# Performance work log

Hardware: AMD Instinct MI355X
Metric: run time of the kernel (lower is better)

Reference implementation:

```python
import jax, jax.numpy as jnp
import numpy as np


def setup_inputs() -> dict:
    key = jax.random.key(0)
    ks = jax.random.split(key, 7)
    B, T, C, H = 4, 4096, 1024, 64
    x = jax.random.normal(ks[0], (B, T, C), dtype=jnp.float32)
    Wq = jax.random.normal(ks[1], (C, H), dtype=jnp.float32) * 0.02
    bq = jax.random.normal(ks[2], (H,), dtype=jnp.float32) * 0.02
    Wk = jax.random.normal(ks[3], (C, H), dtype=jnp.float32) * 0.02
    bk = jax.random.normal(ks[4], (H,), dtype=jnp.float32) * 0.02
    Wv = jax.random.normal(ks[5], (C, H), dtype=jnp.float32) * 0.02
    bv = jax.random.normal(ks[6], (H,), dtype=jnp.float32) * 0.02
    return {"x": x, "Wq": Wq, "bq": bq, "Wk": Wk, "bk": bk, "Wv": Wv, "bv": bv}


def reference(x, Wq, bq, Wk, bk, Wv, bv):
    B, T, C = x.shape
    q = x @ Wq + bq            # [B,T,H]
    k = x @ Wk + bk            # [B,T,H]
    v = x @ Wv + bv            # [B,T,H]
    # NOTE: original scales by C**-0.5 where C = n_embd (input dim), not head_size
    scale = jnp.asarray(C, x.dtype) ** -0.5
    wei = jnp.einsum('bth,bsh->bts', q, k) * scale   # [B,T,T]
    causal = jnp.tril(jnp.ones((T, T), dtype=bool))
    wei = jnp.where(causal, wei, -jnp.inf)
    wei = jax.nn.softmax(wei, axis=-1)
    out = jnp.einsum('bts,bsh->bth', wei, v)         # [B,T,H]
    return out
```

## Files before the change

### kernel.cpp

```cpp
#include <hip/hip_runtime.h>
#include <hip/hip_bf16.h>

#define T_DIM 4096
#define C_DIM 1024
#define H_DIM 64
#define B_DIM 4

typedef __attribute__((ext_vector_type(8))) short short8v;
typedef __attribute__((ext_vector_type(4))) short short4v;
typedef __attribute__((ext_vector_type(4))) float float4v;

__device__ __forceinline__ unsigned short f2bf(float f) {
    __hip_bfloat16 h = __float2bfloat16(f);
    return *reinterpret_cast<unsigned short*>(&h);
}
__device__ __forceinline__ float bf2f(unsigned short u) {
    __hip_bfloat16 h = *reinterpret_cast<__hip_bfloat16*>(&u);
    return __bfloat162float(h);
}

__device__ __forceinline__ int vperm(int t5) {
    return ((t5 & 12) << 1) | (t5 & 3) | ((t5 & 16) >> 2);
}

#define GLL16(gsrc, ldst)                                                         \
    __builtin_amdgcn_global_load_lds(                                             \
        (const __attribute__((address_space(1))) unsigned int*)(gsrc),            \
        (__attribute__((address_space(3))) unsigned int*)(ldst), 16, 0, 0)

__global__ __launch_bounds__(256) void wprep(
    const float* __restrict__ Wq, const float* __restrict__ Wk,
    const float* __restrict__ Wv, unsigned short* __restrict__ wt)
{
    const int tid = blockIdx.x * 256 + threadIdx.x;
    const int k   = tid & 1023;
    const int col = (tid >> 10) & 63;
    const int m   = tid >> 16;
    const float* __restrict__ W = (m == 0) ? Wq : (m == 1) ? Wk : Wv;
    wt[tid] = f2bf(W[k * 64 + col]);
}

__global__ __launch_bounds__(512, 2) void qkv_gemm(
    const float* __restrict__ x, const unsigned short* __restrict__ wt,
    const float* __restrict__ bq, const float* __restrict__ bk,
    const float* __restrict__ bv,
    unsigned short* __restrict__ qb, unsigned short* __restrict__ kmat,
    unsigned short* __restrict__ vP)
{
    __shared__ __align__(16) unsigned char lx[2][16384];
    __shared__ __align__(16) unsigned char lw[2][24576];

    const int t    = threadIdx.x;
    const int w    = t >> 6;
    const int lane = t & 63;
    const int l15  = lane & 15;
    const int g    = lane >> 4;
    const int r0   = blockIdx.x * 64;

    const int xgl = (t & 15) ^ ((t >> 4) & 15);
    const int wgl = (t & 7) ^ ((t >> 3) & 7);

    const unsigned char* __restrict__ xB = (const unsigned char*)x;
    const unsigned char* __restrict__ wB = (const unsigned char*)wt;

#define STAGE(p, kb)                                                              \
    {                                                                             \
        _Pragma("unroll")                                                         \
        for (int i = 0; i < 2; ++i) {                                             \
            const unsigned char* src =                                            \
                xB + (size_t)(r0 + i * 32 + (t >> 4)) * 4096 + (kb) * 256 + xgl * 16; \
            GLL16(src, &lx[p][(i * 512 + t) * 16]);                               \
        }                                                                         \
        _Pragma("unroll")                                                         \
        for (int j = 0; j < 3; ++j) {                                             \
            const unsigned char* src =                                            \
                wB + (size_t)(j * 64 + (t >> 3)) * 2048 + (kb) * 128 + wgl * 16;  \
            GLL16(src, &lw[p][(j * 512 + t) * 16]);                               \
        }                                                                         \
    }

    const int rbase = (w & 3) * 16;
    const int W0    = (w >> 2) * 96;

    float4v acc[6];
#pragma unroll
    for (int cg = 0; cg < 6; ++cg) acc[cg] = (float4v){0.f, 0.f, 0.f, 0.f};

    STAGE(0, 0);
    __syncthreads();

    for (int kb = 0; kb < 16; ++kb) {
        const int p = kb & 1;
        if (kb < 15) STAGE(p ^ 1, kb + 1);

        const int arow = rbase + l15;
        short8v af[2];
#pragma unroll
        for (int ks = 0; ks < 2; ++ks) {
            const int Lg0 = ks * 8 + 2 * g;
            const float4 a0 = *(const float4*)&lx[p][arow * 256 + ((Lg0)     ^ l15) * 16];
            const float4 a1 = *(const float4*)&lx[p][arow * 256 + ((Lg0 + 1) ^ l15) * 16];
            short8v a;
            a[0] = (short)f2bf(a0.x); a[1] = (short)f2bf(a0.y);
            a[2] = (short)f2bf(a0.z); a[3] = (short)f2bf(a0.w);
            a[4] = (short)f2bf(a1.x); a[5] = (short)f2bf(a1.y);
            a[6] = (short)f2bf(a1.z); a[7] = (short)f2bf(a1.w);
            af[ks] = a;
        }

#pragma unroll
        for (int cg = 0; cg < 6; ++cg) {
            const int wrow = W0 + cg * 16 + l15;
#pragma unroll
            for (int ks = 0; ks < 2; ++ks) {
                const int phys = (ks * 4 + g) ^ (l15 & 7);
                const short8v bf = *(const short8v*)&lw[p][wrow * 128 + phys * 16];
                acc[cg] = __builtin_amdgcn_mfma_f32_16x16x32_bf16(af[ks], bf, acc[cg], 0, 0, 0);
            }
        }
        __syncthreads();
    }

    const float qs = 0.03125f * 1.44269504088896f;
#pragma unroll
    for (int cg = 0; cg < 6; ++cg) {
        const int cabs = W0 + cg * 16 + l15;
        const int m    = cabs >> 6;
        const int h    = cabs & 63;
        const float bb = ((m == 0) ? bq : (m == 1) ? bk : bv)[h];
#pragma unroll
        for (int rr = 0; rr < 4; ++rr) {
            const int row = r0 + rbase + 4 * g + rr;
            const float vv = acc[cg][rr] + bb;
            if (m == 0) {
                qb[(size_t)row * 64 + h] = f2bf(vv * qs);
            } else if (m == 1) {
                kmat[(size_t)row * 64 + h] = f2bf(vv);
            } else {
                const int b_i = row >> 12;
                const int tt  = row & 4095;
                const int tp  = (tt & ~31) | vperm(tt & 31);
                vP[((size_t)b_i * 64 + h) * T_DIM + tp] = f2bf(vv);
            }
        }
    }
#undef STAGE
}

__global__ __launch_bounds__(512, 4) void attn_mfma(
    const unsigned short* __restrict__ qb, const unsigned short* __restrict__ kmat,
    const unsigned short* __restrict__ vP, float* __restrict__ out)
{
    __shared__ float partO[8][32][68];
    __shared__ float partl[8][32];

    const int w    = threadIdx.x >> 6;
    const int lane = threadIdx.x & 63;
    const int l15  = lane & 15;
    const int g    = lane >> 4;
    const int i    = blockIdx.x;
    const int p2   = (i & 255) >> 2;
    const int b    = i & 3;
    const int tt   = (i < 256) ? (127 - p2) : p2;
    const int q0   = tt * 32;
    const int n    = tt + 1;

    const unsigned short* __restrict__ qbase = qb + ((size_t)b * T_DIM + q0) * 64;
    short8v qf[2][2];
    qf[0][0] = *(const short8v*)(qbase + (size_t)l15 * 64 + 8 * g);
    qf[0][1] = *(const short8v*)(qbase + (size_t)l15 * 64 + 32 + 8 * g);
    qf[1][0] = *(const short8v*)(qbase + (size_t)(16 + l15) * 64 + 8 * g);
    qf[1][1] = *(const short8v*)(qbase + (size_t)(16 + l15) * 64 + 32 + 8 * g);

    const unsigned short* __restrict__ kbase = kmat + (size_t)b * T_DIM * 64;
    const unsigned short* __restrict__ vbase = vP + (size_t)b * 64 * T_DIM;

    float4v acc[2][4];
#pragma unroll
    for (int qt = 0; qt < 2; ++qt)
#pragma unroll
        for (int f = 0; f < 4; ++f) acc[qt][f] = (float4v){0.f, 0.f, 0.f, 0.f};
    float lsum[2] = {0.f, 0.f};

    const int rem = n & 7;
    const int cnt = (n >> 3) + (w < rem ? 1 : 0);
    const int st  = w * (n >> 3) + (w < rem ? w : rem);

    for (int s = 0; s < cnt; ++s) {
        const int kv0 = (st + s) * 32;

        const unsigned short* kr0 = kbase + (size_t)(kv0 + l15) * 64 + 8 * g;
        const unsigned short* kr1 = kr0 + 16 * 64;
        const short8v ka0 = *(const short8v*)kr0;
        const short8v ka1 = *(const short8v*)(kr0 + 32);
        const short8v ka2 = *(const short8v*)kr1;
        const short8v ka3 = *(const short8v*)(kr1 + 32);

        short8v vb4[4];
#pragma unroll
        for (int f = 0; f < 4; ++f)
            vb4[f] = *(const short8v*)(
                vbase + (size_t)(f * 16 + l15) * T_DIM + kv0 + 8 * g);

#pragma unroll
        for (int qt = 0; qt < 2; ++qt) {
            const float4v z = (float4v){0.f, 0.f, 0.f, 0.f};
            float4v slo = __builtin_amdgcn_mfma_f32_16x16x32_bf16(ka0, qf[qt][0], z, 0, 0, 0);
            slo = __builtin_amdgcn_mfma_f32_16x16x32_bf16(ka1, qf[qt][1], slo, 0, 0, 0);
            float4v shi = __builtin_amdgcn_mfma_f32_16x16x32_bf16(ka2, qf[qt][0], z, 0, 0, 0);
            shi = __builtin_amdgcn_mfma_f32_16x16x32_bf16(ka3, qf[qt][1], shi, 0, 0, 0);

            const int qabs = q0 + 16 * qt + l15;
            short8v pa;
            float ls = 0.f;
#pragma unroll
            for (int r = 0; r < 4; ++r) {
                const int kvlo = kv0 + 4 * g + r;
                const float plo = (kvlo <= qabs) ? exp2f(slo[r]) : 0.f;
                const float phi = (kvlo + 16 <= qabs) ? exp2f(shi[r]) : 0.f;
                const unsigned short ulo = f2bf(plo);
                const unsigned short uhi = f2bf(phi);
                pa[r]     = (short)ulo;
                pa[4 + r] = (short)uhi;
                ls += bf2f(ulo) + bf2f(uhi);
            }
            lsum[qt] += ls;
#pragma unroll
            for (int f = 0; f < 4; ++f)
                acc[qt][f] = __builtin_amdgcn_mfma_f32_16x16x32_bf16(pa, vb4[f], acc[qt][f], 0, 0, 0);
        }
    }

#pragma unroll
    for (int qt = 0; qt < 2; ++qt) {
        lsum[qt] += __shfl_xor(lsum[qt], 16);
        lsum[qt] += __shfl_xor(lsum[qt], 32);
    }

#pragma unroll
    for (int qt = 0; qt < 2; ++qt)
#pragma unroll
        for (int f = 0; f < 4; ++f)
#pragma unroll
            for (int r = 0; r < 4; ++r)
                partO[w][16 * qt + 4 * g + r][16 * f + l15] = acc[qt][f][r];
    if (g == 0) {
        partl[w][l15]      = lsum[0];
        partl[w][16 + l15] = lsum[1];
    }
    __syncthreads();

    const int row = threadIdx.x >> 4;
    const int c0  = (threadIdx.x & 15) * 4;
    float lt = 0.f;
#pragma unroll
    for (int ww = 0; ww < 8; ++ww) lt += partl[ww][row];
    const float inv = 1.f / lt;
    float4 o = make_float4(0.f, 0.f, 0.f, 0.f);
#pragma unroll
    for (int ww = 0; ww < 8; ++ww) {
        const float4 s = *(const float4*)&partO[ww][row][c0];
        o.x += s.x; o.y += s.y; o.z += s.z; o.w += s.w;
    }
    o.x *= inv; o.y *= inv; o.z *= inv; o.w *= inv;
    *(float4*)(out + ((size_t)b * T_DIM + q0 + row) * 64 + c0) = o;
}

extern "C" void kernel_launch(void* const* d_in, const int* in_sizes, int n_in,
                              void* d_out, int out_size, void* d_ws, size_t ws_size,
                              hipStream_t stream) {
    const float* x  = (const float*)d_in[0];
    const float* Wq = (const float*)d_in[1];
    const float* bq = (const float*)d_in[2];
    const float* Wk = (const float*)d_in[3];
    const float* bk = (const float*)d_in[4];
    const float* Wv = (const float*)d_in[5];
    const float* bv = (const float*)d_in[6];
    float* out = (float*)d_out;

    const size_t rows = (size_t)B_DIM * T_DIM;
    char* ws = (char*)d_ws;
    unsigned short* qb   = (unsigned short*)ws;
    unsigned short* kmat = qb + rows * H_DIM;
    unsigned short* vP   = kmat + rows * H_DIM;
    unsigned short* wt   = vP + rows * H_DIM;

    wprep<<<768, 256, 0, stream>>>(Wq, Wk, Wv, wt);
    qkv_gemm<<<256, 512, 0, stream>>>(x, wt, bq, bk, bv, qb, kmat, vP);
    attn_mfma<<<512, 512, 0, stream>>>(qb, kmat, vP, out);
}
```

Before: 65.97 us.

## Restructure QKV GEMM with 32x32 MFMA and split-K, pipeline K loads in attention

The weight-prep kernel now transposes through a shared-memory tile, using coalesced float4 reads and 16-byte writes across far fewer blocks. The QKV GEMM converts x to bf16 once while staging it into LDS, which halves the x tile. It switches to 32x32x16 MFMA with a two-way split-K across waves and reduces the partial sums through LDS. The attention kernel double-buffers K fragments across iterations, skips the causal mask on fully unmasked tiles, sums fp32 probabilities directly, and raises wave priority around MFMA groups. The trade-offs are more register pressure, an extra LDS reduction step, and a row-sum that no longer exactly matches the bf16-rounded weights.

```diff
diff --git a/kernel.cpp b/kernel.cpp
--- a/kernel.cpp
+++ b/kernel.cpp
@@ -9,14 +9,11 @@
 typedef __attribute__((ext_vector_type(8))) short short8v;
 typedef __attribute__((ext_vector_type(4))) short short4v;
 typedef __attribute__((ext_vector_type(4))) float float4v;
+typedef __attribute__((ext_vector_type(16))) float float16v;
 
 __device__ __forceinline__ unsigned short f2bf(float f) {
     __hip_bfloat16 h = __float2bfloat16(f);
     return *reinterpret_cast<unsigned short*>(&h);
-}
-__device__ __forceinline__ float bf2f(unsigned short u) {
-    __hip_bfloat16 h = *reinterpret_cast<__hip_bfloat16*>(&u);
-    return __bfloat162float(h);
 }
 
 __device__ __forceinline__ int vperm(int t5) {
@@ -32,12 +29,31 @@
     const float* __restrict__ Wq, const float* __restrict__ Wk,
     const float* __restrict__ Wv, unsigned short* __restrict__ wt)
 {
-    const int tid = blockIdx.x * 256 + threadIdx.x;
-    const int k   = tid & 1023;
-    const int col = (tid >> 10) & 63;
-    const int m   = tid >> 16;
+    __shared__ float tile[64][65];
+    const int t  = threadIdx.x;
+    const int m  = blockIdx.x >> 4;
+    const int k0 = (blockIdx.x & 15) * 64;
     const float* __restrict__ W = (m == 0) ? Wq : (m == 1) ? Wk : Wv;
-    wt[tid] = f2bf(W[k * 64 + col]);
+
+    const int kr = t >> 4, c4 = (t & 15) * 4;
+#pragma unroll
+    for (int j = 0; j < 4; ++j) {
+        const int row = kr + j * 16;
+        const float4 v = *(const float4*)(W + (size_t)(k0 + row) * 64 + c4);
+        tile[row][c4 + 0] = v.x; tile[row][c4 + 1] = v.y;
+        tile[row][c4 + 2] = v.z; tile[row][c4 + 3] = v.w;
+    }
+    __syncthreads();
+
+    const int col = t >> 2, q = t & 3;
+    short8v s0, s1;
+#pragma unroll
+    for (int j = 0; j < 8; ++j) s0[j] = (short)f2bf(tile[q * 16 + j][col]);
+#pragma unroll
+    for (int j = 0; j < 8; ++j) s1[j] = (short)f2bf(tile[q * 16 + 8 + j][col]);
+    unsigned short* dst = wt + (size_t)(m * 64 + col) * 1024 + k0 + q * 16;
+    *(short8v*)dst = s0;
+    *(short8v*)(dst + 8) = s1;
 }
 
 __global__ __launch_bounds__(512, 2) void qkv_gemm(
@@ -47,104 +63,136 @@
     unsigned short* __restrict__ qb, unsigned short* __restrict__ kmat,
     unsigned short* __restrict__ vP)
 {
-    __shared__ __align__(16) unsigned char lx[2][16384];
+    __shared__ __align__(16) unsigned char lx[2][8192];
     __shared__ __align__(16) unsigned char lw[2][24576];
 
     const int t    = threadIdx.x;
+    const int lane = t & 63;
     const int w    = t >> 6;
-    const int lane = t & 63;
-    const int l15  = lane & 15;
-    const int g    = lane >> 4;
+    const int l31  = lane & 31;
+    const int hi   = lane >> 5;
     const int r0   = blockIdx.x * 64;
 
-    const int xgl = (t & 15) ^ ((t >> 4) & 15);
-    const int wgl = (t & 7) ^ ((t >> 3) & 7);
-
-    const unsigned char* __restrict__ xB = (const unsigned char*)x;
+    const int rg  = w & 1;
+    const int cgr = (w >> 1) & 1;
+    const int kh  = w >> 2;
+
+    const int srow  = t >> 3;
+    const int soct  = t & 7;
+    const int sphys = soct ^ (srow & 7);
+    const float* __restrict__ xsrc = x + (size_t)(r0 + srow) * C_DIM + soct * 8;
+    const int wgs = (t & 7) ^ ((t >> 3) & 7);
     const unsigned char* __restrict__ wB = (const unsigned char*)wt;
 
-#define STAGE(p, kb)                                                              \
+    float16v acc[3];
+#pragma unroll
+    for (int cg = 0; cg < 3; ++cg)
+#pragma unroll
+        for (int e = 0; e < 16; ++e) acc[cg][e] = 0.f;
+
+#define WSTAGE(p, kb)                                                             \
     {                                                                             \
         _Pragma("unroll")                                                         \
-        for (int i = 0; i < 2; ++i) {                                             \
-            const unsigned char* src =                                            \
-                xB + (size_t)(r0 + i * 32 + (t >> 4)) * 4096 + (kb) * 256 + xgl * 16; \
-            GLL16(src, &lx[p][(i * 512 + t) * 16]);                               \
-        }                                                                         \
-        _Pragma("unroll")                                                         \
-        for (int j = 0; j < 3; ++j) {                                             \
-            const unsigned char* src =                                            \
-                wB + (size_t)(j * 64 + (t >> 3)) * 2048 + (kb) * 128 + wgl * 16;  \
-            GLL16(src, &lw[p][(j * 512 + t) * 16]);                               \
-        }                                                                         \
-    }
-
-    const int rbase = (w & 3) * 16;
-    const int W0    = (w >> 2) * 96;
-
-    float4v acc[6];
-#pragma unroll
-    for (int cg = 0; cg < 6; ++cg) acc[cg] = (float4v){0.f, 0.f, 0.f, 0.f};
-
-    STAGE(0, 0);
+        for (int i = 0; i < 3; ++i)                                               \
+            GLL16(wB + (size_t)(i * 64 + (t >> 3)) * 2048 + (kb) * 128 + wgs * 16,\
+                  &lw[p][(i * 512 + t) * 16]);                                    \
+    }
+
+    {
+        const float4 a0 = *(const float4*)(xsrc);
+        const float4 a1 = *(const float4*)(xsrc + 4);
+        WSTAGE(0, 0);
+        short8v xs;
+        xs[0] = (short)f2bf(a0.x); xs[1] = (short)f2bf(a0.y);
+        xs[2] = (short)f2bf(a0.z); xs[3] = (short)f2bf(a0.w);
+        xs[4] = (short)f2bf(a1.x); xs[5] = (short)f2bf(a1.y);
+        xs[6] = (short)f2bf(a1.z); xs[7] = (short)f2bf(a1.w);
+        *(short8v*)&lx[0][srow * 128 + sphys * 16] = xs;
+    }
     __syncthreads();
+
+    const int arow = rg * 32 + l31;
+    const int axor = arow & 7;
 
     for (int kb = 0; kb < 16; ++kb) {
         const int p = kb & 1;
-        if (kb < 15) STAGE(p ^ 1, kb + 1);
-
-        const int arow = rbase + l15;
+        float4 na = {0,0,0,0}, nb = {0,0,0,0};
+        if (kb < 15) {
+            na = *(const float4*)(xsrc + (kb + 1) * 64);
+            nb = *(const float4*)(xsrc + (kb + 1) * 64 + 4);
+            WSTAGE(p ^ 1, kb + 1);
+        }
+
         short8v af[2];
 #pragma unroll
         for (int ks = 0; ks < 2; ++ks) {
-            const int Lg0 = ks * 8 + 2 * g;
-            const float4 a0 = *(const float4*)&lx[p][arow * 256 + ((Lg0)     ^ l15) * 16];
-            const float4 a1 = *(const float4*)&lx[p][arow * 256 + ((Lg0 + 1) ^ l15) * 16];
-            short8v a;
-            a[0] = (short)f2bf(a0.x); a[1] = (short)f2bf(a0.y);
-            a[2] = (short)f2bf(a0.z); a[3] = (short)f2bf(a0.w);
-            a[4] = (short)f2bf(a1.x); a[5] = (short)f2bf(a1.y);
-            a[6] = (short)f2bf(a1.z); a[7] = (short)f2bf(a1.w);
-            af[ks] = a;
-        }
-
-#pragma unroll
-        for (int cg = 0; cg < 6; ++cg) {
-            const int wrow = W0 + cg * 16 + l15;
+            const int kg = kh * 4 + ks * 2 + hi;
+            af[ks] = *(const short8v*)&lx[p][arow * 128 + (kg ^ axor) * 16];
+        }
+#pragma unroll
+        for (int cg = 0; cg < 3; ++cg) {
+            const int col = cgr * 96 + cg * 32 + l31;
 #pragma unroll
             for (int ks = 0; ks < 2; ++ks) {
-                const int phys = (ks * 4 + g) ^ (l15 & 7);
-                const short8v bf = *(const short8v*)&lw[p][wrow * 128 + phys * 16];
-                acc[cg] = __builtin_amdgcn_mfma_f32_16x16x32_bf16(af[ks], bf, acc[cg], 0, 0, 0);
+                const int kg = kh * 4 + ks * 2 + hi;
+                const short8v bf =
+                    *(const short8v*)&lw[p][col * 128 + ((kg ^ (col & 7))) * 16];
+                acc[cg] = __builtin_amdgcn_mfma_f32_32x32x16_bf16(af[ks], bf, acc[cg], 0, 0, 0);
             }
         }
+
+        if (kb < 15) {
+            short8v xs;
+            xs[0] = (short)f2bf(na.x); xs[1] = (short)f2bf(na.y);
+            xs[2] = (short)f2bf(na.z); xs[3] = (short)f2bf(na.w);
+            xs[4] = (short)f2bf(nb.x); xs[5] = (short)f2bf(nb.y);
+            xs[6] = (short)f2bf(nb.z); xs[7] = (short)f2bf(nb.w);
+            *(short8v*)&lx[p ^ 1][srow * 128 + sphys * 16] = xs;
+        }
         __syncthreads();
     }
 
-    const float qs = 0.03125f * 1.44269504088896f;
-#pragma unroll
-    for (int cg = 0; cg < 6; ++cg) {
-        const int cabs = W0 + cg * 16 + l15;
-        const int m    = cabs >> 6;
-        const int h    = cabs & 63;
-        const float bb = ((m == 0) ? bq : (m == 1) ? bk : bv)[h];
-#pragma unroll
-        for (int rr = 0; rr < 4; ++rr) {
-            const int row = r0 + rbase + 4 * g + rr;
-            const float vv = acc[cg][rr] + bb;
-            if (m == 0) {
-                qb[(size_t)row * 64 + h] = f2bf(vv * qs);
-            } else if (m == 1) {
-                kmat[(size_t)row * 64 + h] = f2bf(vv);
-            } else {
-                const int b_i = row >> 12;
-                const int tt  = row & 4095;
-                const int tp  = (tt & ~31) | vperm(tt & 31);
-                vP[((size_t)b_i * 64 + h) * T_DIM + tp] = f2bf(vv);
+    float* comm = (float*)lw;
+    if (kh == 1) {
+        const int base = ((w - 4) * 64 + lane) * 48;
+#pragma unroll
+        for (int cg = 0; cg < 3; ++cg)
+#pragma unroll
+            for (int e = 0; e < 16; ++e) comm[base + cg * 16 + e] = acc[cg][e];
+    }
+    __syncthreads();
+    if (kh == 0) {
+        const int base = (w * 64 + lane) * 48;
+#pragma unroll
+        for (int cg = 0; cg < 3; ++cg)
+#pragma unroll
+            for (int e = 0; e < 16; ++e) acc[cg][e] += comm[base + cg * 16 + e];
+
+        const float qs = 0.03125f * 1.44269504088896f;
+#pragma unroll
+        for (int cg = 0; cg < 3; ++cg) {
+            const int cabs = cgr * 96 + cg * 32 + l31;
+            const int m    = cabs >> 6;
+            const int h    = cabs & 63;
+            const float bb = ((m == 0) ? bq : (m == 1) ? bk : bv)[h];
+#pragma unroll
+            for (int reg = 0; reg < 16; ++reg) {
+                const int row = r0 + rg * 32 + (reg & 3) + 8 * (reg >> 2) + 4 * hi;
+                const float vv = acc[cg][reg] + bb;
+                if (m == 0) {
+                    qb[(size_t)row * 64 + h] = f2bf(vv * qs);
+                } else if (m == 1) {
+                    kmat[(size_t)row * 64 + h] = f2bf(vv);
+                } else {
+                    const int b_i = row >> 12;
+                    const int tt  = row & 4095;
+                    const int tp  = (tt & ~31) | vperm(tt & 31);
+                    vP[((size_t)b_i * 64 + h) * T_DIM + tp] = f2bf(vv);
+                }
             }
         }
     }
-#undef STAGE
+#undef WSTAGE
 }
 
 __global__ __launch_bounds__(512, 4) void attn_mfma(
@@ -186,50 +234,84 @@
     const int cnt = (n >> 3) + (w < rem ? 1 : 0);
     const int st  = w * (n >> 3) + (w < rem ? w : rem);
 
-    for (int s = 0; s < cnt; ++s) {
-        const int kv0 = (st + s) * 32;
-
-        const unsigned short* kr0 = kbase + (size_t)(kv0 + l15) * 64 + 8 * g;
-        const unsigned short* kr1 = kr0 + 16 * 64;
-        const short8v ka0 = *(const short8v*)kr0;
-        const short8v ka1 = *(const short8v*)(kr0 + 32);
-        const short8v ka2 = *(const short8v*)kr1;
-        const short8v ka3 = *(const short8v*)(kr1 + 32);
-
-        short8v vb4[4];
-#pragma unroll
-        for (int f = 0; f < 4; ++f)
-            vb4[f] = *(const short8v*)(
-                vbase + (size_t)(f * 16 + l15) * T_DIM + kv0 + 8 * g);
-
-#pragma unroll
-        for (int qt = 0; qt < 2; ++qt) {
-            const float4v z = (float4v){0.f, 0.f, 0.f, 0.f};
-            float4v slo = __builtin_amdgcn_mfma_f32_16x16x32_bf16(ka0, qf[qt][0], z, 0, 0, 0);
-            slo = __builtin_amdgcn_mfma_f32_16x16x32_bf16(ka1, qf[qt][1], slo, 0, 0, 0);
-            float4v shi = __builtin_amdgcn_mfma_f32_16x16x32_bf16(ka2, qf[qt][0], z, 0, 0, 0);
-            shi = __builtin_amdgcn_mfma_f32_16x16x32_bf16(ka3, qf[qt][1], shi, 0, 0, 0);
-
-            const int qabs = q0 + 16 * qt + l15;
-            short8v pa;
-            float ls = 0.f;
-#pragma unroll
-            for (int r = 0; r < 4; ++r) {
-                const int kvlo = kv0 + 4 * g + r;
-                const float plo = (kvlo <= qabs) ? exp2f(slo[r]) : 0.f;
-                const float phi = (kvlo + 16 <= qabs) ? exp2f(shi[r]) : 0.f;
-                const unsigned short ulo = f2bf(plo);
-                const unsigned short uhi = f2bf(phi);
-                pa[r]     = (short)ulo;
-                pa[4 + r] = (short)uhi;
-                ls += bf2f(ulo) + bf2f(uhi);
-            }
-            lsum[qt] += ls;
-#pragma unroll
-            for (int f = 0; f < 4; ++f)
-                acc[qt][f] = __builtin_amdgcn_mfma_f32_16x16x32_bf16(pa, vb4[f], acc[qt][f], 0, 0, 0);
-        }
-    }
+#define LOADK(KA, KV0)                                                        \
+    {                                                                         \
+        const unsigned short* kr_ = kbase + (size_t)((KV0) + l15) * 64 + 8*g; \
+        KA[0] = *(const short8v*)kr_;                                         \
+        KA[1] = *(const short8v*)(kr_ + 32);                                  \
+        KA[2] = *(const short8v*)(kr_ + 1024);                                \
+        KA[3] = *(const short8v*)(kr_ + 1056);                                \
+    }
+#define LOADV(KV0)                                                            \
+    {                                                                         \
+        _Pragma("unroll")                                                     \
+        for (int f_ = 0; f_ < 4; ++f_)                                        \
+            vb[f_] = *(const short8v*)(vbase +                                \
+                (size_t)(f_ * 16 + l15) * T_DIM + (KV0) + 8 * g);             \
+    }
+#define STEP(KA, KV0)                                                         \
+    {                                                                         \
+        _Pragma("unroll")                                                     \
+        for (int qt = 0; qt < 2; ++qt) {                                      \
+            const float4v z_ = (float4v){0.f, 0.f, 0.f, 0.f};                 \
+            __builtin_amdgcn_s_setprio(1);                                    \
+            float4v slo = __builtin_amdgcn_mfma_f32_16x16x32_bf16(KA[0], qf[qt][0], z_, 0, 0, 0); \
+            slo = __builtin_amdgcn_mfma_f32_16x16x32_bf16(KA[1], qf[qt][1], slo, 0, 0, 0); \
+            float4v shi = __builtin_amdgcn_mfma_f32_16x16x32_bf16(KA[2], qf[qt][0], z_, 0, 0, 0); \
+            shi = __builtin_amdgcn_mfma_f32_16x16x32_bf16(KA[3], qf[qt][1], shi, 0, 0, 0); \
+            __builtin_amdgcn_s_setprio(0);                                    \
+            short8v pa;                                                       \
+            float ls = 0.f;                                                   \
+            if ((KV0) + 31 <= q0 + 16 * qt) {                                 \
+                _Pragma("unroll")                                             \
+                for (int r = 0; r < 4; ++r) {                                 \
+                    const float plo = exp2f(slo[r]);                          \
+                    const float phi = exp2f(shi[r]);                          \
+                    pa[r]     = (short)f2bf(plo);                             \
+                    pa[4 + r] = (short)f2bf(phi);                             \
+                    ls += plo + phi;                                          \
+                }                                                             \
+            } else {                                                          \
+                const int qabs = q0 + 16 * qt + l15;                          \
+                _Pragma("unroll")                                             \
+                for (int r = 0; r < 4; ++r) {                                 \
+                    const int kvlo = (KV0) + 4 * g + r;                       \
+                    const float plo = (kvlo <= qabs) ? exp2f(slo[r]) : 0.f;   \
+                    const float phi = (kvlo + 16 <= qabs) ? exp2f(shi[r]) : 0.f; \
+                    pa[r]     = (short)f2bf(plo);                             \
+                    pa[4 + r] = (short)f2bf(phi);                             \
+                    ls += plo + phi;                                          \
+                }                                                             \
+            }                                                                 \
+            lsum[qt] += ls;                                                   \
+            __builtin_amdgcn_s_setprio(1);                                    \
+            _Pragma("unroll")                                                 \
+            for (int f = 0; f < 4; ++f)                                       \
+                acc[qt][f] = __builtin_amdgcn_mfma_f32_16x16x32_bf16(pa, vb[f], acc[qt][f], 0, 0, 0); \
+            __builtin_amdgcn_s_setprio(0);                                    \
+        }                                                                     \
+    }
+
+    short8v kaA[4], kaB[4], vb[4];
+    if (cnt > 0) {
+        LOADK(kaA, st * 32);
+        int s = 0;
+        while (true) {
+            const int kv0 = (st + s) * 32;
+            LOADV(kv0);
+            if (s + 1 < cnt) LOADK(kaB, (st + s + 1) * 32);
+            STEP(kaA, kv0);
+            if (++s >= cnt) break;
+            const int kv1 = (st + s) * 32;
+            LOADV(kv1);
+            if (s + 1 < cnt) LOADK(kaA, (st + s + 1) * 32);
+            STEP(kaB, kv1);
+            if (++s >= cnt) break;
+        }
+    }
+#undef LOADK
+#undef LOADV
+#undef STEP
 
 #pragma unroll
     for (int qt = 0; qt < 2; ++qt) {
@@ -285,7 +367,7 @@
     unsigned short* vP   = kmat + rows * H_DIM;
     unsigned short* wt   = vP + rows * H_DIM;
 
-    wprep<<<768, 256, 0, stream>>>(Wq, Wk, Wv, wt);
+    wprep<<<48, 256, 0, stream>>>(Wq, Wk, Wv, wt);
     qkv_gemm<<<256, 512, 0, stream>>>(x, wt, bq, bk, bv, qb, kmat, vP);
     attn_mfma<<<512, 512, 0, stream>>>(qb, kmat, vP, out);
 }
```

After: 87.47 us. 1.33x slower.
